# Kernel optimization log

Hardware: AMD Instinct MI355X
Metric: run time of the kernel (lower is better)

Reference implementation:

```python
import jax, jax.numpy as jnp
import numpy as np

N, DIM = 32768, 2048
SPARSITY = 0.05
K = max(1, int(N * SPARSITY))  # 1638


def setup_inputs() -> dict:
    key = jax.random.key(0)
    ks = jax.random.split(key, 6)
    s = 1.0 / np.sqrt(DIM)
    return {
        "x": jax.random.normal(ks[0], (N, DIM), dtype=jnp.float32),
        "W1": jax.random.uniform(ks[1], (DIM, DIM), jnp.float32, -s, s),
        "b1": jax.random.uniform(ks[2], (DIM,), jnp.float32, -s, s),
        "W2": jax.random.uniform(ks[3], (DIM, DIM), jnp.float32, -s, s),
        "b2": jax.random.uniform(ks[4], (DIM,), jnp.float32, -s, s),
        "Wg": jax.random.uniform(ks[5], (DIM,), jnp.float32, -s, s),
        "bg": jnp.zeros((), jnp.float32),
    }


def reference(x, W1, b1, W2, b2, Wg, bg):
    # gate scores per row: [N]
    gate_scores = x @ Wg + bg
    # select top-k rows (k is static)
    _, top_idx = jax.lax.top_k(gate_scores, K)
    # gather active rows and run the 2-layer MLP only on them
    active_x = x[top_idx]                                   # [K, DIM]
    h = jax.nn.relu(active_x @ W1 + b1)
    active_out = h @ W2 + b2                                # [K, DIM]
    # scatter results back into a zero output; row order is irrelevant
    output = jnp.zeros_like(x).at[top_idx].set(active_out)
    mask = jnp.zeros((x.shape[0],), x.dtype).at[top_idx].set(1.0)
    return output, mask
```

## Files before the change

kernel.cpp:

```cpp
#include <hip/hip_runtime.h>

#define N_ROWS 32768
#define DIM    2048
#define KSEL   1638
#define MPAD   1664
#define GTILE  416

typedef __attribute__((ext_vector_type(4))) float          f32x4;
typedef __attribute__((ext_vector_type(4))) unsigned short us4;
typedef __attribute__((ext_vector_type(8))) unsigned short us8;
typedef __bf16 bf16x8 __attribute__((ext_vector_type(8)));

__device__ __forceinline__ unsigned short f2bf(float f) {
    unsigned u = __float_as_uint(f);
    u += 0x7FFFu + ((u >> 16) & 1u);
    return (unsigned short)(u >> 16);
}

__device__ __forceinline__ void gload_lds16(const void* g, void* l) {
    __builtin_amdgcn_global_load_lds(
        (const __attribute__((address_space(1))) unsigned int*)(uintptr_t)g,
        (__attribute__((address_space(3))) unsigned int*)(uintptr_t)l, 16, 0, 0);
}


__global__ __launch_bounds__(256) void gate_k(const float* __restrict__ x,
                                              const float* __restrict__ Wg,
                                              const float* __restrict__ bg,
                                              float* __restrict__ scores) {
    const int t = threadIdx.x;
    const int lane = t & 63, wid = t >> 6;
    const int row = blockIdx.x * 4 + wid;
    const float* xr = x + (size_t)row * DIM;
    float acc = 0.f;
#pragma unroll
    for (int i = 0; i < 8; ++i) {
        const int c = i * 256 + lane * 4;
        f32x4 a = __builtin_nontemporal_load((const f32x4*)&xr[c]);
        f32x4 w = *(const f32x4*)&Wg[c];
#pragma unroll
        for (int j = 0; j < 4; ++j) acc = fmaf(a[j], w[j], acc);
    }
#pragma unroll
    for (int off = 32; off >= 1; off >>= 1) acc += __shfl_down(acc, off);
    if (lane == 0) scores[row] = acc + bg[0];
}

__device__ __forceinline__ void wave_find(const unsigned* hist, int per,
                                          unsigned need, int lane,
                                          int* ob, unsigned* oabove) {
    unsigned g = 0;
    for (int i = 0; i < per; ++i) g += hist[lane * per + i];
    unsigned s = g;
#pragma unroll
    for (int d = 1; d < 64; d <<= 1) {
        unsigned v = (unsigned)__shfl_down((int)s, d);
        if (lane + d < 64) s += v;
    }
    const unsigned long long m = __ballot(s >= need);
    const int gb = 63 - __builtin_clzll(m);
    const unsigned above_g = (unsigned)__shfl((int)(s - g), gb);
    const unsigned need2 = need - above_g;
    unsigned h = (lane < per) ? hist[gb * per + lane] : 0u;
    unsigned s2 = h;
#pragma unroll
    for (int d = 1; d < 64; d <<= 1) {
        unsigned v = (unsigned)__shfl_down((int)s2, d);
        if (lane + d < 64) s2 += v;
    }
    const unsigned long long m2 = __ballot(s2 >= need2);
    const int bb = 63 - __builtin_clzll(m2);
    const unsigned above_b = (unsigned)__shfl((int)(s2 - h), bb);
    *ob = gb * per + bb;
    *oabove = above_g + above_b;
}

__global__ __launch_bounds__(1024) void selconvt_k(const float* __restrict__ scores,
                                                   int* __restrict__ sel,
                                                   const float* __restrict__ W1,
                                                   const float* __restrict__ W2,
                                                   unsigned short* __restrict__ W1t,
                                                   unsigned short* __restrict__ W2t) {
    __shared__ unsigned short tile[4][64][72];
    __shared__ unsigned hist[2048];
    __shared__ unsigned bcb, bcn;
    const int t = threadIdx.x;

    if (blockIdx.x > 0) {
        const int sb = t >> 8, t8 = t & 255;
        const int cb = (blockIdx.x - 1) * 4 + sb;
        const int z = cb >> 10;
        const int rem = cb & 1023;
        const int k0 = (rem & 31) * 64;
        const int n0 = (rem >> 5) * 64;
        const float* W = z ? W2 : W1;
        unsigned short* Wt = z ? W2t : W1t;
        {
            const int r = t8 >> 4, c = (t8 & 15) * 4;
#pragma unroll
            for (int p = 0; p < 4; ++p) {
                const int rr = p * 16 + r;
                f32x4 v = *(const f32x4*)&W[(size_t)(k0 + rr) * DIM + n0 + c];
#pragma unroll
                for (int j = 0; j < 4; ++j) tile[sb][rr][c + j] = f2bf(v[j]);
            }
        }
        __syncthreads();
        {
            const int n = t8 >> 4, kk = (t8 & 15) * 4;
#pragma unroll
            for (int p = 0; p < 4; ++p) {
                const int nn = p * 16 + n;
                us4 o;
#pragma unroll
                for (int j = 0; j < 4; ++j) o[j] = tile[sb][kk + j][nn];
                *(us4*)&Wt[(size_t)(n0 + nn) * DIM + k0 + kk] = o;
            }
        }
        return;
    }

    const int lane = t & 63;
    unsigned key[32];
#pragma unroll
    for (int i = 0; i < 8; ++i) {
        f32x4 v = *(const f32x4*)&scores[t * 32 + i * 4];
#pragma unroll
        for (int j = 0; j < 4; ++j) {
            unsigned u = __float_as_uint(v[j]);
            u = (u & 0x80000000u) ? ~u : (u | 0x80000000u);
            key[i * 4 + j] = u;
        }
    }
    hist[t] = 0u; hist[t + 1024] = 0u;
    __syncthreads();
#pragma unroll
    for (int i = 0; i < 32; ++i) atomicAdd(&hist[key[i] >> 21], 1u);
    __syncthreads();
    if (t < 64) {
        int b; unsigned ab;
        wave_find(hist, 32, KSEL, lane, &b, &ab);
        if (t == 0) { bcb = (unsigned)b; bcn = KSEL - ab; }
    }
    __syncthreads();
    const unsigned p1 = bcb; const unsigned need2 = bcn;
    hist[t] = 0u; hist[t + 1024] = 0u;
    __syncthreads();
#pragma unroll
    for (int i = 0; i < 32; ++i)
        if ((key[i] >> 21) == p1) atomicAdd(&hist[(key[i] >> 10) & 0x7FFu], 1u);
    __syncthreads();
    if (t < 64) {
        int b; unsigned ab;
        wave_find(hist, 32, need2, lane, &b, &ab);
        if (t == 0) { bcb = (unsigned)b; bcn = need2 - ab; }
    }
    __syncthreads();
    const unsigned p2 = (p1 << 11) | bcb; const unsigned need3 = bcn;
    hist[t] = 0u; hist[t + 1024] = 0u;
    __syncthreads();
#pragma unroll
    for (int i = 0; i < 32; ++i)
        if ((key[i] >> 10) == p2) atomicAdd(&hist[key[i] & 0x3FFu], 1u);
    __syncthreads();
    if (t < 64) {
        int b; unsigned ab;
        wave_find(hist, 16, need3, lane, &b, &ab);
        if (t == 0) bcb = (unsigned)b;
    }
    __syncthreads();
    const unsigned kv = (p2 << 10) | bcb;

    __shared__ unsigned ctr, ectr;
    __shared__ int eq[256];
    if (t == 0) { ctr = 0; ectr = 0; }
    __syncthreads();
#pragma unroll
    for (int i = 0; i < 32; ++i) {
        const unsigned k = key[i];
        if (k > kv) {
            unsigned p = atomicAdd(&ctr, 1u);
            sel[p] = t * 32 + i;
        } else if (k == kv) {
            unsigned p = atomicAdd(&ectr, 1u);
            if (p < 256u) eq[p] = t * 32 + i;
        }
    }
    __syncthreads();
    if (t == 0) {
        const int C = (int)ctr;
        const int R = KSEL - C;
        const int E = (int)(ectr < 256u ? ectr : 256u);
        for (int r = 0; r < R; ++r) {
            int mi = r;
            for (int j = r + 1; j < E; ++j)
                if (eq[j] < eq[mi]) mi = j;
            int tmp = eq[r]; eq[r] = eq[mi]; eq[mi] = tmp;
            sel[C + r] = eq[r];
        }
    }
}

__global__ __launch_bounds__(256) void gather_k(const float* __restrict__ x,
                                                const int* __restrict__ sel,
                                                unsigned short* __restrict__ Abf,
                                                float* __restrict__ mask) {
    const int b = blockIdx.x, t = threadIdx.x;
    unsigned short* dst = Abf + (size_t)b * DIM + t * 8;
    if (b < KSEL) {
        const int src = sel[b];
        if (t == 0) mask[src] = 1.0f;
        const float* xr = x + (size_t)src * DIM + t * 8;
        f32x4 v0 = *(const f32x4*)xr;
        f32x4 v1 = *(const f32x4*)(xr + 4);
        us8 o;
#pragma unroll
        for (int j = 0; j < 4; ++j) { o[j] = f2bf(v0[j]); o[j + 4] = f2bf(v1[j]); }
        *(us8*)dst = o;
    } else {
        us8 z = {};
        *(us8*)dst = z;
    }
}

template <int EPI>
__global__ __launch_bounds__(256, 2) void gemm_k(const unsigned short* __restrict__ A,
                                                 const unsigned short* __restrict__ Bt,
                                                 const float* __restrict__ bias,
                                                 unsigned short* __restrict__ Hout,
                                                 float* __restrict__ Cout,
                                                 const int* __restrict__ sel) {
    __shared__ unsigned short lA[2][128 * 64];
    __shared__ unsigned short lB[2][64 * 64];
    const int t = threadIdx.x;
    const int lane = t & 63;
    const int wid = t >> 6;
    const int swz = (blockIdx.x & 7) * 52 + (blockIdx.x >> 3);
    const int m0 = (swz % 13) * 128;
    const int n0 = (swz / 13) * 64;
    const int wm = (wid >> 1) * 64;
    const int wn = (wid & 1) * 32;

    f32x4 acc[4][2] = {};

    const unsigned short *gA[4], *gB[2];
    int la[4], lb[2];
#pragma unroll
    for (int i = 0; i < 4; ++i) {
        const int e = t + i * 256, r = e >> 3;
        gA[i] = A + (size_t)(m0 + r) * DIM + ((e & 7) ^ (r & 7)) * 8;
        la[i] = e * 8;
    }
#pragma unroll
    for (int i = 0; i < 2; ++i) {
        const int e = t + i * 256, r = e >> 3;
        gB[i] = Bt + (size_t)(n0 + r) * DIM + ((e & 7) ^ (r & 7)) * 8;
        lb[i] = e * 8;
    }

    const int pc0 = (((lane >> 4) + 0) ^ (lane & 7)) * 8;
    const int pc1 = (((lane >> 4) + 4) ^ (lane & 7)) * 8;
    const int aob = (wm + (lane & 15)) * 64;
    const int bob = (wn + (lane & 15)) * 64;

#pragma unroll
    for (int i = 0; i < 4; ++i) gload_lds16(gA[i], &lA[0][la[i]]);
#pragma unroll
    for (int i = 0; i < 2; ++i) gload_lds16(gB[i], &lB[0][lb[i]]);
    __syncthreads();

    int cur = 0;
    for (int k0 = 0; k0 < DIM; k0 += 64) {
        if (k0 + 64 < DIM) {
            const int nxt = cur ^ 1, kn = k0 + 64;
#pragma unroll
            for (int i = 0; i < 4; ++i) gload_lds16(gA[i] + kn, &lA[nxt][la[i]]);
#pragma unroll
            for (int i = 0; i < 2; ++i) gload_lds16(gB[i] + kn, &lB[nxt][lb[i]]);
        }
        bf16x8 af0[4], af1[4], bf0[2], bf1[2];
#pragma unroll
        for (int mf = 0; mf < 4; ++mf) {
            af0[mf] = *(const bf16x8*)&lA[cur][aob + mf * 1024 + pc0];
            af1[mf] = *(const bf16x8*)&lA[cur][aob + mf * 1024 + pc1];
        }
#pragma unroll
        for (int nf = 0; nf < 2; ++nf) {
            bf0[nf] = *(const bf16x8*)&lB[cur][bob + nf * 1024 + pc0];
            bf1[nf] = *(const bf16x8*)&lB[cur][bob + nf * 1024 + pc1];
        }
#pragma unroll
        for (int mf = 0; mf < 4; ++mf)
#pragma unroll
            for (int nf = 0; nf < 2; ++nf)
                acc[mf][nf] = __builtin_amdgcn_mfma_f32_16x16x32_bf16(
                    af0[mf], bf0[nf], acc[mf][nf], 0, 0, 0);
#pragma unroll
        for (int mf = 0; mf < 4; ++mf)
#pragma unroll
            for (int nf = 0; nf < 2; ++nf)
                acc[mf][nf] = __builtin_amdgcn_mfma_f32_16x16x32_bf16(
                    af1[mf], bf1[nf], acc[mf][nf], 0, 0, 0);
        __syncthreads();
        cur ^= 1;
    }

#pragma unroll
    for (int mf = 0; mf < 4; ++mf) {
        const int rbase = m0 + wm + mf * 16 + (lane >> 4) * 4;
#pragma unroll
        for (int nf = 0; nf < 2; ++nf) {
            const int col = n0 + wn + nf * 16 + (lane & 15);
            const float bv = bias[col];
            if (EPI == 0) {
#pragma unroll
                for (int j = 0; j < 4; ++j) {
                    float v = acc[mf][nf][j] + bv;
                    v = fmaxf(v, 0.f);
                    Hout[(size_t)(rbase + j) * DIM + col] = f2bf(v);
                }
            } else {
#pragma unroll
                for (int j = 0; j < 4; ++j) {
                    const int r = rbase + j;
                    if (r < KSEL) {
                        __builtin_nontemporal_store(
                            acc[mf][nf][j] + bv,
                            &Cout[(size_t)sel[r] * DIM + col]);
                    }
                }
            }
        }
    }
}

extern "C" void kernel_launch(void* const* d_in, const int* in_sizes, int n_in,
                              void* d_out, int out_size, void* d_ws, size_t ws_size,
                              hipStream_t stream) {
    const float* x  = (const float*)d_in[0];
    const float* W1 = (const float*)d_in[1];
    const float* b1 = (const float*)d_in[2];
    const float* W2 = (const float*)d_in[3];
    const float* b2 = (const float*)d_in[4];
    const float* Wg = (const float*)d_in[5];
    const float* bg = (const float*)d_in[6];
    float* out  = (float*)d_out;
    float* mask = out + (size_t)N_ROWS * DIM;

    char* w = (char*)d_ws;
    float* scores = (float*)w;           w += (size_t)N_ROWS * 4;
    int* sel = (int*)w;                  w += 2048 * 4;
    unsigned short* Abf = (unsigned short*)w;  w += (size_t)MPAD * DIM * 2;
    unsigned short* Hbf = (unsigned short*)w;  w += (size_t)MPAD * DIM * 2;
    unsigned short* W1t = (unsigned short*)w;  w += (size_t)DIM * DIM * 2;
    unsigned short* W2t = (unsigned short*)w;  w += (size_t)DIM * DIM * 2;

    hipLaunchKernelGGL(gate_k, dim3(N_ROWS / 4), dim3(256), 0, stream,
                       x, Wg, bg, scores);
    hipLaunchKernelGGL(selconvt_k, dim3(513), dim3(1024), 0, stream,
                       scores, sel, W1, W2, W1t, W2t);
    hipLaunchKernelGGL(gather_k, dim3(MPAD), dim3(256), 0, stream, x, sel, Abf, mask);
    hipLaunchKernelGGL((gemm_k<0>), dim3(GTILE), dim3(256), 0, stream,
                       Abf, W1t, b1, Hbf, (float*)nullptr, (const int*)nullptr);
    hipLaunchKernelGGL((gemm_k<1>), dim3(GTILE), dim3(256), 0, stream,
                       Hbf, W2t, b2, (unsigned short*)nullptr, out, sel);
}
```

Measured before the change: 114.9 us.

## Split K across warp pairs in GEMM and reduce partial sums through LDS

```diff
diff --git a/kernel.cpp b/kernel.cpp
--- a/kernel.cpp
+++ b/kernel.cpp
@@ -238,10 +238,10 @@
     const int swz = (blockIdx.x & 7) * 52 + (blockIdx.x >> 3);
     const int m0 = (swz % 13) * 128;
     const int n0 = (swz / 13) * 64;
-    const int wm = (wid >> 1) * 64;
-    const int wn = (wid & 1) * 32;
-
-    f32x4 acc[4][2] = {};
+    const int wm = (wid & 1) * 64;
+    const int kh4 = (wid >> 1) * 4;
+
+    f32x4 acc[4][4] = {};
 
     const unsigned short *gA[4], *gB[2];
     int la[4], lb[2];
@@ -258,10 +258,9 @@
         lb[i] = e * 8;
     }
 
-    const int pc0 = (((lane >> 4) + 0) ^ (lane & 7)) * 8;
-    const int pc1 = (((lane >> 4) + 4) ^ (lane & 7)) * 8;
+    const int pc = (((lane >> 4) + kh4) ^ (lane & 7)) * 8;
     const int aob = (wm + (lane & 15)) * 64;
-    const int bob = (wn + (lane & 15)) * 64;
+    const int bob = (lane & 15) * 64;
 
 #pragma unroll
     for (int i = 0; i < 4; ++i) gload_lds16(gA[i], &lA[0][la[i]]);
@@ -278,39 +277,44 @@
 #pragma unroll
             for (int i = 0; i < 2; ++i) gload_lds16(gB[i] + kn, &lB[nxt][lb[i]]);
         }
-        bf16x8 af0[4], af1[4], bf0[2], bf1[2];
-#pragma unroll
-        for (int mf = 0; mf < 4; ++mf) {
-            af0[mf] = *(const bf16x8*)&lA[cur][aob + mf * 1024 + pc0];
-            af1[mf] = *(const bf16x8*)&lA[cur][aob + mf * 1024 + pc1];
-        }
-#pragma unroll
-        for (int nf = 0; nf < 2; ++nf) {
-            bf0[nf] = *(const bf16x8*)&lB[cur][bob + nf * 1024 + pc0];
-            bf1[nf] = *(const bf16x8*)&lB[cur][bob + nf * 1024 + pc1];
-        }
+        bf16x8 af[4], bfr[4];
 #pragma unroll
         for (int mf = 0; mf < 4; ++mf)
-#pragma unroll
-            for (int nf = 0; nf < 2; ++nf)
+            af[mf] = *(const bf16x8*)&lA[cur][aob + mf * 1024 + pc];
+#pragma unroll
+        for (int nf = 0; nf < 4; ++nf)
+            bfr[nf] = *(const bf16x8*)&lB[cur][bob + nf * 1024 + pc];
+#pragma unroll
+        for (int mf = 0; mf < 4; ++mf)
+#pragma unroll
+            for (int nf = 0; nf < 4; ++nf)
                 acc[mf][nf] = __builtin_amdgcn_mfma_f32_16x16x32_bf16(
-                    af0[mf], bf0[nf], acc[mf][nf], 0, 0, 0);
-#pragma unroll
-        for (int mf = 0; mf < 4; ++mf)
-#pragma unroll
-            for (int nf = 0; nf < 2; ++nf)
-                acc[mf][nf] = __builtin_amdgcn_mfma_f32_16x16x32_bf16(
-                    af1[mf], bf1[nf], acc[mf][nf], 0, 0, 0);
+                    af[mf], bfr[nf], acc[mf][nf], 0, 0, 0);
         __syncthreads();
         cur ^= 1;
     }
 
+    float* fbuf = (float*)&lA[0][0];
+    const int half = wid & 1;
+    if (wid >> 1) {
+#pragma unroll
+        for (int mf = 0; mf < 4; ++mf)
+#pragma unroll
+            for (int nf = 0; nf < 4; ++nf)
+                *(f32x4*)&fbuf[half * 4096 + (mf * 4 + nf) * 256 + lane * 4] =
+                    acc[mf][nf];
+    }
+    __syncthreads();
+    if (wid >> 1) return;
+
 #pragma unroll
     for (int mf = 0; mf < 4; ++mf) {
         const int rbase = m0 + wm + mf * 16 + (lane >> 4) * 4;
 #pragma unroll
-        for (int nf = 0; nf < 2; ++nf) {
-            const int col = n0 + wn + nf * 16 + (lane & 15);
+        for (int nf = 0; nf < 4; ++nf) {
+            acc[mf][nf] += *(const f32x4*)&fbuf[half * 4096 + (mf * 4 + nf) * 256 +
+                                                lane * 4];
+            const int col = n0 + nf * 16 + (lane & 15);
             const float bv = bias[col];
             if (EPI == 0) {
 #pragma unroll
```

New measurement: 116.2 us. About the same (+1.1%).
